# Kernel optimization log

Measured on AMD Instinct MI355X. Metric: run time of the kernel, lower is better.

## Reference

```python
import jax, jax.numpy as jnp
import numpy as np

B, T, H, FUT = 256, 512, 128, 512


def setup_inputs() -> dict:
    key = jax.random.key(0)
    ks = jax.random.split(key, 24)
    s = 1.0 / np.sqrt(H)

    def u(k, shape, scale):
        return jax.random.uniform(k, shape, jnp.float32, -scale, scale)

    inp = {
        "input": jax.random.normal(ks[0], (B, T), jnp.float32),
        "future": FUT,
        # LSTMCell 1 (input size 1)
        "Wih1": u(ks[1], (4 * H, 1), s), "Whh1": u(ks[2], (4 * H, H), s),
        "bih1": u(ks[3], (4 * H,), s), "bhh1": u(ks[4], (4 * H,), s),
        # LSTMCell 2
        "Wih2": u(ks[5], (4 * H, H), s), "Whh2": u(ks[6], (4 * H, H), s),
        "bih2": u(ks[7], (4 * H,), s), "bhh2": u(ks[8], (4 * H,), s),
        # LSTMCell 3
        "Wih3": u(ks[9], (4 * H, H), s), "Whh3": u(ks[10], (4 * H, H), s),
        "bih3": u(ks[11], (4 * H,), s), "bhh3": u(ks[12], (4 * H,), s),
        # MultiheadAttention packed in-proj (q,k,v) and out-proj
        "in_proj_w": u(ks[13], (3 * H, H), s), "in_proj_b": u(ks[14], (3 * H,), s),
        "out_w": u(ks[15], (H, H), s), "out_b": u(ks[16], (H,), s),
        # final Linear(H, 1)
        "lin_w": u(ks[17], (1, H), s), "lin_b": u(ks[18], (1,), s),
    }
    return inp


def _lstm_cell(x, h, c, Wih, Whh, bih, bhh):
    # torch LSTMCell gate order: i, f, g, o
    g = x @ Wih.T + h @ Whh.T + (bih + bhh)
    i, f, gg, o = jnp.split(g, 4, axis=-1)
    c_new = jax.nn.sigmoid(f) * c + jax.nn.sigmoid(i) * jnp.tanh(gg)
    h_new = jax.nn.sigmoid(o) * jnp.tanh(c_new)
    return h_new, c_new


def _forward(input, Wih1, Whh1, bih1, bhh1, Wih2, Whh2, bih2, bhh2,
             Wih3, Whh3, bih3, bhh3, in_proj_w, in_proj_b, out_w, out_b,
             lin_w, lin_b, future):
    hd = in_proj_w.shape[1]
    # seq_len == 1 attention: softmax over a single key is 1, so
    # attn_output = out_proj(v_proj(h3)); q/k play no role in the output.
    Wv = in_proj_w[2 * hd:]
    bv = in_proj_b[2 * hd:]

    def head(h3):
        attn = (h3 @ Wv.T + bv) @ out_w.T + out_b
        return attn @ lin_w.T + lin_b  # [B, 1]

    def step(states, x_t):
        h1, c1, h2, c2, h3, c3 = states
        h1, c1 = _lstm_cell(x_t, h1, c1, Wih1, Whh1, bih1, bhh1)
        h2, c2 = _lstm_cell(h1, h2, c2, Wih2, Whh2, bih2, bhh2)
        h3, c3 = _lstm_cell(h2, h3, c3, Wih3, Whh3, bih3, bhh3)
        return (h1, c1, h2, c2, h3, c3), head(h3)

    n = input.shape[0]
    z = jnp.zeros((n, hd), input.dtype)
    init = (z, z, z, z, z, z)

    xs = input.T[:, :, None]  # [T, B, 1]
    states, outs = jax.lax.scan(lambda s, x: step(s, x), init, xs)

    def fstep(carry, _):
        st, out = carry
        st, out = step(st, out)
        return (st, out), out

    (_, _), fouts = jax.lax.scan(fstep, (states, outs[-1]), None, length=future)
    all_outs = jnp.concatenate([outs, fouts], axis=0)  # [T+future, B, 1]
    return all_outs[..., 0].T  # [B, T+future]


def reference(input, Wih1, Whh1, bih1, bhh1, Wih2, Whh2, bih2, bhh2,
              Wih3, Whh3, bih3, bhh3, in_proj_w, in_proj_b, out_w, out_b,
              lin_w, lin_b, future):
    return _forward(input, Wih1, Whh1, bih1, bhh1, Wih2, Whh2, bih2, bhh2,
                    Wih3, Whh3, bih3, bhh3, in_proj_w, in_proj_b, out_w,
                    out_b, lin_w, lin_b, future)
```

## Files before the change

kernel.cpp:

```cpp
#include <hip/hip_runtime.h>


typedef _Float16 f16;
typedef _Float16 f16x2 __attribute__((ext_vector_type(2)));
typedef unsigned int u32;

#define T_IN 512
#define T_TOT 1024
#define NBLK 128

__device__ __forceinline__ f16x2 u2h(u32 u) { return __builtin_bit_cast(f16x2, u); }

__device__ __forceinline__ float fdot2f(f16x2 a, f16x2 b, float c) {
#if __has_builtin(__builtin_amdgcn_fdot2)
  return __builtin_amdgcn_fdot2(a, b, c, false);
#else
  return c + (float)a[0] * (float)b[0] + (float)a[1] * (float)b[1];
#endif
}

__device__ __forceinline__ float frcp(float x) {
#if __has_builtin(__builtin_amdgcn_rcpf)
  return __builtin_amdgcn_rcpf(x);
#else
  return 1.f / x;
#endif
}
__device__ __forceinline__ float fsigm(float x) { return frcp(1.f + __expf(-x)); }
__device__ __forceinline__ float ftanh(float x) { return 1.f - 2.f * frcp(1.f + __expf(2.f * x)); }

#define DOT4(acc, w, hv)                     \
  do {                                       \
    f16x2 _h = u2h(hv);                      \
    acc[0] = fdot2f(u2h((w).x), _h, acc[0]); \
    acc[1] = fdot2f(u2h((w).y), _h, acc[1]); \
    acc[2] = fdot2f(u2h((w).z), _h, acc[2]); \
    acc[3] = fdot2f(u2h((w).w), _h, acc[3]); \
  } while (0)

__global__ void pack_cat(u32* dst, const float* A, const float* Bm, int Pa, int P) {
  int tid = blockIdx.x * 256 + threadIdx.x;
  if (tid >= P * 512) return;
  int g = tid & 3;
  int idx = (tid >> 2) & 127;
  int p = tid >> 9;
  int j = g * 128 + idx;
  const float* src;
  int k;
  if (p < Pa) { src = A; k = 2 * p; } else { src = Bm; k = 2 * (p - Pa); }
  union { f16 h[2]; u32 u; } cv;
  cv.h[0] = (f16)src[j * 128 + k];
  cv.h[1] = (f16)src[j * 128 + k + 1];
  dst[tid] = cv.u;
}

__global__ void pack1(u32* dst, const float* Whh1) {
  int tid = blockIdx.x * 256 + threadIdx.x;
  if (tid >= 64 * 512) return;
  int g = tid & 3;
  int idx = (tid >> 2) & 127;
  int p = tid >> 9;
  int j = g * 128 + idx;
  union { f16 h[2]; u32 u; } cv;
  cv.h[0] = (f16)Whh1[j * 128 + 2 * p];
  cv.h[1] = (f16)Whh1[j * 128 + 2 * p + 1];
  dst[(p * 128 + (idx ^ (2 * (p >> 4)))) * 4 + g] = cv.u;
}

__global__ void pack3(u32* dst, const float* Wih3, const float* Whh3) {
  int tid = blockIdx.x * 256 + threadIdx.x;
  if (tid >= 128 * 512) return;
  int g = tid & 3;
  int u4i = tid >> 2;
  int kq = u4i & 3;
  int idx = (u4i >> 2) & 127;
  int i = u4i >> 9;
  int p = (i < 16) ? (64 + kq * 16 + i) : (kq * 16 + (i - 16));
  int j = g * 128 + idx;
  const float* src = (p < 64) ? Wih3 : Whh3;
  int k = (p < 64) ? 2 * p : 2 * (p - 64);
  union { f16 h[2]; u32 u; } cv;
  cv.h[0] = (f16)src[j * 128 + k];
  cv.h[1] = (f16)src[j * 128 + k + 1];
  dst[tid] = cv.u;
}

__global__ void prep_cons(float* cons, const float* a1, const float* b1,
                          const float* a2, const float* b2,
                          const float* a3, const float* b3, const float* wih1) {
  int tid = blockIdx.x * 256 + threadIdx.x;
  if (tid >= 2048) return;
  int gg = tid >> 9, g = (tid >> 7) & 3, idx = tid & 127;
  int j = g * 128 + idx;
  float v;
  if (gg == 0) v = a1[j] + b1[j];
  else if (gg == 1) v = a2[j] + b2[j];
  else if (gg == 2) v = a3[j] + b3[j];
  else v = wih1[j];
  cons[tid] = v;
}

__global__ void head_fold(float* cons, const float* lin_w, const float* out_w,
                          const float* Wv, const float* bv,
                          const float* out_b, const float* lin_b) {
  __shared__ float wlo[128];
  __shared__ float pr[128];
  int j = threadIdx.x;
  float s = 0.f;
  for (int k = 0; k < 128; ++k) s += lin_w[k] * out_w[k * 128 + j];
  wlo[j] = s;
  __syncthreads();
  float t = 0.f;
  for (int k = 0; k < 128; ++k) t += wlo[k] * Wv[k * 128 + j];
  cons[2048 + j] = t;
  pr[j] = s * bv[j] + lin_w[j] * out_b[j];
  __syncthreads();
  if (j == 0) {
    float b = lin_b[0];
    for (int k = 0; k < 128; ++k) b += pr[k];
    cons[2176] = b;
  }
}

__global__ __launch_bounds__(512, 1) void pendulum_persist(
    const float* __restrict__ input, const uint4* __restrict__ WT1g,
    const uint4* __restrict__ WT2, const uint4* __restrict__ WT3r,
    const float* __restrict__ consG, float* __restrict__ out) {
  __shared__ __align__(16) uint4 w1lds[8192];
  __shared__ __align__(16) f16 h1b[2][2][128];
  __shared__ __align__(16) f16 h2b[2][2][128];
  __shared__ __align__(16) f16 h3b[2][128];
  __shared__ float consL[2180];
  __shared__ float redp[2][8];

  const int t = threadIdx.x;
  const int idx = t >> 2;
  const int kq = t & 3;
  const int row0 = blockIdx.x * 2, row1 = row0 + 1;

  for (int e = t; e < 8192; e += 512) w1lds[e] = WT1g[e];
  for (int e = t; e < 2177; e += 512) consL[e] = consG[e];
  if (t < 128) {
    h1b[0][0][t] = (f16)0.f; h1b[0][1][t] = (f16)0.f;
    h1b[1][0][t] = (f16)0.f; h1b[1][1][t] = (f16)0.f;
    h2b[0][0][t] = (f16)0.f; h2b[0][1][t] = (f16)0.f;
    h2b[1][0][t] = (f16)0.f; h2b[1][1][t] = (f16)0.f;
    h3b[0][t] = (f16)0.f;    h3b[1][t] = (f16)0.f;
  }

  uint4 w2r[32];
#pragma unroll
  for (int j = 0; j < 32; ++j) w2r[j] = WT2[(kq * 32 + j) * 128 + idx];

  const uint4* W3p = WT3r + t;
  const uint4* w1p = w1lds + kq * 2048 + (idx ^ (2 * kq));

  float c1a = 0.f, c1b = 0.f, c2a = 0.f, c2b = 0.f, c3a = 0.f, c3b = 0.f;
  float y0 = 0.f, y1 = 0.f;
  __syncthreads();
  const float beffv = consL[2176];

  {
    float x0 = input[row0 * T_IN], x1 = input[row1 * T_IN];
    if (kq == 0) {
      float b0 = consL[idx], b1v = consL[128 + idx], b2v = consL[256 + idx],
            b3v = consL[384 + idx];
      float w0 = consL[1536 + idx], w1w = consL[1664 + idx],
            w2w = consL[1792 + idx], w3w = consL[1920 + idx];
      {
        float ig = fsigm(b0 + x0 * w0), fg = fsigm(b1v + x0 * w1w);
        float gg = ftanh(b2v + x0 * w2w), og = fsigm(b3v + x0 * w3w);
        (void)fg; c1a = ig * gg; h1b[0][0][idx] = (f16)(og * ftanh(c1a));
      }
      {
        float ig = fsigm(b0 + x1 * w0), fg = fsigm(b1v + x1 * w1w);
        float gg = ftanh(b2v + x1 * w2w), og = fsigm(b3v + x1 * w3w);
        (void)fg; c1b = ig * gg; h1b[0][1][idx] = (f16)(og * ftanh(c1b));
      }
    }
    __syncthreads();
  }

  uint4 ring[8];
#pragma unroll
  for (int c = 0; c < 8; ++c) ring[c] = W3p[c * 512];

  for (int s = 0; s < T_TOT; ++s) {
    const int par = s & 1;
    const int xi = (s + 1 < T_IN) ? (s + 1) : 0;
    float xl0 = input[row0 * T_IN + xi];
    float xl1 = input[row1 * T_IN + xi];

    const uint4* hL2r0 = (kq < 2)
        ? (const uint4*)&h1b[par][0][0] + kq * 8
        : (const uint4*)&h2b[par ^ 1][0][0] + (kq - 2) * 8;
    const uint4* hL2r1 = (kq < 2)
        ? (const uint4*)&h1b[par][1][0] + kq * 8
        : (const uint4*)&h2b[par ^ 1][1][0] + (kq - 2) * 8;
    const uint4* h3r0 = (const uint4*)&h3b[0][0] + kq * 4;
    const uint4* h3r1 = (const uint4*)&h3b[1][0] + kq * 4;

    float a2r0[4] = {0, 0, 0, 0}, a2r1[4] = {0, 0, 0, 0};
    float a3r0[4] = {0, 0, 0, 0}, a3r1[4] = {0, 0, 0, 0};

    uint4 E0, E1;
#pragma unroll
    for (int q = 0; q < 8; ++q) {
      uint4 H0 = hL2r0[q], H1 = hL2r1[q];
      u32 e0[4] = {H0.x, H0.y, H0.z, H0.w};
      u32 e1[4] = {H1.x, H1.y, H1.z, H1.w};
#pragma unroll
      for (int e = 0; e < 4; ++e) {
        uint4 w = w2r[q * 4 + e];
        DOT4(a2r0, w, e0[e]);
        DOT4(a2r1, w, e1[e]);
      }
      if ((q & 1) == 0) { E0 = h3r0[q >> 1]; E1 = h3r1[q >> 1]; }
      {
        uint4 w = ring[(2 * q) & 7];
        ring[(2 * q) & 7] = W3p[(2 * q + 8) * 512];
        u32 h0 = (q & 1) ? E0.z : E0.x, h1v = (q & 1) ? E1.z : E1.x;
        DOT4(a3r0, w, h0);
        DOT4(a3r1, w, h1v);
      }
      {
        uint4 w = ring[(2 * q + 1) & 7];
        ring[(2 * q + 1) & 7] = W3p[(2 * q + 9) * 512];
        u32 h0 = (q & 1) ? E0.w : E0.y, h1v = (q & 1) ? E1.w : E1.y;
        DOT4(a3r0, w, h0);
        DOT4(a3r1, w, h1v);
      }
    }

#pragma unroll
    for (int g = 0; g < 4; ++g) {
      a2r0[g] += __shfl_xor(a2r0[g], 1, 64); a2r0[g] += __shfl_xor(a2r0[g], 2, 64);
      a2r1[g] += __shfl_xor(a2r1[g], 1, 64); a2r1[g] += __shfl_xor(a2r1[g], 2, 64);
    }
    if (kq == 0) {
      float b0 = consL[512 + idx], b1v = consL[640 + idx],
            b2v = consL[768 + idx], b3v = consL[896 + idx];
      {
        float ig = fsigm(a2r0[0] + b0), fg = fsigm(a2r0[1] + b1v);
        float gg = ftanh(a2r0[2] + b2v), og = fsigm(a2r0[3] + b3v);
        c2a = fg * c2a + ig * gg;
        h2b[par][0][idx] = (f16)(og * ftanh(c2a));
      }
      {
        float ig = fsigm(a2r1[0] + b0), fg = fsigm(a2r1[1] + b1v);
        float gg = ftanh(a2r1[2] + b2v), og = fsigm(a2r1[3] + b3v);
        c2b = fg * c2b + ig * gg;
        h2b[par][1][idx] = (f16)(og * ftanh(c2b));
      }
    }
    asm volatile("s_waitcnt lgkmcnt(0)\n\ts_barrier" ::: "memory");

    const uint4* hLTr0 = (const uint4*)&h2b[par][0][0] + kq * 4;
    const uint4* hLTr1 = (const uint4*)&h2b[par][1][0] + kq * 4;
    const uint4* h1r0 = (const uint4*)&h1b[par][0][0] + kq * 4;
    const uint4* h1r1 = (const uint4*)&h1b[par][1][0] + kq * 4;

    float a1r0[4] = {0, 0, 0, 0}, a1r1[4] = {0, 0, 0, 0};
    uint4 L0, L1v, F0, F1;
#pragma unroll
    for (int q = 0; q < 8; ++q) {
      if ((q & 1) == 0) {
        L0 = hLTr0[q >> 1]; L1v = hLTr1[q >> 1];
        F0 = h1r0[q >> 1];  F1 = h1r1[q >> 1];
      }
      {
        uint4 w = ring[(2 * q) & 7];
        ring[(2 * q) & 7] = W3p[(((16 + 2 * q) + 8) & 31) * 512];
        u32 h0 = (q & 1) ? L0.z : L0.x, h1x = (q & 1) ? L1v.z : L1v.x;
        DOT4(a3r0, w, h0);
        DOT4(a3r1, w, h1x);
      }
      {
        uint4 w = ring[(2 * q + 1) & 7];
        ring[(2 * q + 1) & 7] = W3p[(((17 + 2 * q) + 8) & 31) * 512];
        u32 h0 = (q & 1) ? L0.w : L0.y, h1x = (q & 1) ? L1v.w : L1v.y;
        DOT4(a3r0, w, h0);
        DOT4(a3r1, w, h1x);
      }
      {
        uint4 w = w1p[(2 * q) * 128];
        u32 h0 = (q & 1) ? F0.z : F0.x, h1x = (q & 1) ? F1.z : F1.x;
        DOT4(a1r0, w, h0);
        DOT4(a1r1, w, h1x);
      }
      {
        uint4 w = w1p[(2 * q + 1) * 128];
        u32 h0 = (q & 1) ? F0.w : F0.y, h1x = (q & 1) ? F1.w : F1.y;
        DOT4(a1r0, w, h0);
        DOT4(a1r1, w, h1x);
      }
    }

#pragma unroll
    for (int g = 0; g < 4; ++g) {
      a3r0[g] += __shfl_xor(a3r0[g], 1, 64); a3r0[g] += __shfl_xor(a3r0[g], 2, 64);
      a3r1[g] += __shfl_xor(a3r1[g], 1, 64); a3r1[g] += __shfl_xor(a3r1[g], 2, 64);
      a1r0[g] += __shfl_xor(a1r0[g], 1, 64); a1r0[g] += __shfl_xor(a1r0[g], 2, 64);
      a1r1[g] += __shfl_xor(a1r1[g], 1, 64); a1r1[g] += __shfl_xor(a1r1[g], 2, 64);
    }

    float p0 = 0.f, p1 = 0.f;
    if (kq == 0) {
      float b0 = consL[1024 + idx], b1v = consL[1152 + idx],
            b2v = consL[1280 + idx], b3v = consL[1408 + idx];
      float weffr = consL[2048 + idx];
      {
        float ig = fsigm(a3r0[0] + b0), fg = fsigm(a3r0[1] + b1v);
        float gg = ftanh(a3r0[2] + b2v), og = fsigm(a3r0[3] + b3v);
        c3a = fg * c3a + ig * gg;
        float h3 = og * ftanh(c3a);
        h3b[0][idx] = (f16)h3;
        p0 = weffr * h3;
      }
      {
        float ig = fsigm(a3r1[0] + b0), fg = fsigm(a3r1[1] + b1v);
        float gg = ftanh(a3r1[2] + b2v), og = fsigm(a3r1[3] + b3v);
        c3b = fg * c3b + ig * gg;
        float h3 = og * ftanh(c3b);
        h3b[1][idx] = (f16)h3;
        p1 = weffr * h3;
      }
    }
#pragma unroll
    for (int k = 1; k < 64; k <<= 1) {
      p0 += __shfl_xor(p0, k, 64);
      p1 += __shfl_xor(p1, k, 64);
    }
    if ((t & 63) == 0) { redp[0][t >> 6] = p0; redp[1][t >> 6] = p1; }
    asm volatile("s_waitcnt lgkmcnt(0)\n\ts_barrier" ::: "memory");

    y0 = beffv; y1 = beffv;
#pragma unroll
    for (int w8 = 0; w8 < 8; ++w8) { y0 += redp[0][w8]; y1 += redp[1][w8]; }
    if (t == 0) out[row0 * T_TOT + s] = y0;
    else if (t == 1) out[row1 * T_TOT + s] = y1;

    float xv0 = (s + 1 < T_IN) ? xl0 : y0;
    float xv1 = (s + 1 < T_IN) ? xl1 : y1;
    if (kq == 0) {
      float b0 = consL[idx], b1v = consL[128 + idx], b2v = consL[256 + idx],
            b3v = consL[384 + idx];
      float w0 = consL[1536 + idx], w1w = consL[1664 + idx],
            w2w = consL[1792 + idx], w3w = consL[1920 + idx];
      {
        float ig = fsigm(a1r0[0] + b0 + xv0 * w0), fg = fsigm(a1r0[1] + b1v + xv0 * w1w);
        float gg = ftanh(a1r0[2] + b2v + xv0 * w2w), og = fsigm(a1r0[3] + b3v + xv0 * w3w);
        c1a = fg * c1a + ig * gg;
        h1b[par ^ 1][0][idx] = (f16)(og * ftanh(c1a));
      }
      {
        float ig = fsigm(a1r1[0] + b0 + xv1 * w0), fg = fsigm(a1r1[1] + b1v + xv1 * w1w);
        float gg = ftanh(a1r1[2] + b2v + xv1 * w2w), og = fsigm(a1r1[3] + b3v + xv1 * w3w);
        c1b = fg * c1b + ig * gg;
        h1b[par ^ 1][1][idx] = (f16)(og * ftanh(c1b));
      }
    }
    asm volatile("s_waitcnt lgkmcnt(0)\n\ts_barrier" ::: "memory");
  }
}

extern "C" void kernel_launch(void* const* d_in, const int* in_sizes, int n_in,
                              void* d_out, int out_size, void* d_ws, size_t ws_size,
                              hipStream_t stream) {
  const float* input = (const float*)d_in[0];
  const float* Wih1 = (const float*)d_in[2];
  const float* Whh1 = (const float*)d_in[3];
  const float* bih1 = (const float*)d_in[4];
  const float* bhh1 = (const float*)d_in[5];
  const float* Wih2 = (const float*)d_in[6];
  const float* Whh2 = (const float*)d_in[7];
  const float* bih2 = (const float*)d_in[8];
  const float* bhh2 = (const float*)d_in[9];
  const float* Wih3 = (const float*)d_in[10];
  const float* Whh3 = (const float*)d_in[11];
  const float* bih3 = (const float*)d_in[12];
  const float* bhh3 = (const float*)d_in[13];
  const float* in_proj_w = (const float*)d_in[14];
  const float* in_proj_b = (const float*)d_in[15];
  const float* out_w = (const float*)d_in[16];
  const float* out_b = (const float*)d_in[17];
  const float* lin_w = (const float*)d_in[18];
  const float* lin_b = (const float*)d_in[19];

  char* ws = (char*)d_ws;
  u32* WT1 = (u32*)(ws + (0 << 10));
  u32* WT2 = (u32*)(ws + (128 << 10));
  u32* WT3r = (u32*)(ws + (384 << 10));
  float* consG = (float*)(ws + (640 << 10));

  pack1<<<128, 256, 0, stream>>>(WT1, Whh1);
  pack_cat<<<256, 256, 0, stream>>>(WT2, Wih2, Whh2, 64, 128);
  pack3<<<256, 256, 0, stream>>>(WT3r, Wih3, Whh3);
  prep_cons<<<8, 256, 0, stream>>>(consG, bih1, bhh1, bih2, bhh2, bih3, bhh3, Wih1);
  head_fold<<<1, 128, 0, stream>>>(consG, lin_w, out_w,
                                   in_proj_w + 2 * 128 * 128, in_proj_b + 256,
                                   out_b, lin_b);

  pendulum_persist<<<NBLK, 512, 0, stream>>>(
      input, (const uint4*)WT1, (const uint4*)WT2, (const uint4*)WT3r,
      consG, (float*)d_out);
}
```

Before: 10.21 ms.

## Stream layer-2 weights from global via unified ring instead of register-resident

Layer-2 weights no longer sit in 32 registers per thread. They are interleaved with layer-3 weights into a single packed stream, read each step through a 16-entry register ring prefetch. The layer-1 LDS layout also changes to a per-thread linear order without the XOR swizzle. The aim is to free registers and unify the load schedule. The cost is roughly doubled global/L2 weight traffic per step on a latency-bound recurrent loop, and possible LDS bank conflicts from the unswizzled layout.

After: 12.79 ms. 25.2% more time.

```diff
diff --git a/kernel.cpp b/kernel.cpp
--- a/kernel.cpp
+++ b/kernel.cpp
@@ -38,50 +38,48 @@
     acc[3] = fdot2f(u2h((w).w), _h, acc[3]); \
   } while (0)
 
-__global__ void pack_cat(u32* dst, const float* A, const float* Bm, int Pa, int P) {
+__global__ void pack_stream(u32* dst, const float* Wih2, const float* Whh2,
+                            const float* Wih3, const float* Whh3) {
   int tid = blockIdx.x * 256 + threadIdx.x;
-  if (tid >= P * 512) return;
+  if (tid >= 64 * 512 * 4) return;
   int g = tid & 3;
-  int idx = (tid >> 2) & 127;
-  int p = tid >> 9;
+  int t = (tid >> 2) & 511;
+  int s = tid >> 11;
+  int idx = t >> 2, kq = t & 3;
+  const float* src;
+  int p;
+  if (s < 48) {
+    int q = s / 6, rmd = s % 6;
+    if (rmd < 4) {
+      p = kq * 32 + 4 * q + rmd;
+      if (p < 64) { src = Wih2; } else { src = Whh2; p -= 64; }
+    } else {
+      p = kq * 16 + 2 * q + (rmd - 4);
+      src = Whh3;
+    }
+  } else {
+    p = kq * 16 + (s - 48);
+    src = Wih3;
+  }
   int j = g * 128 + idx;
-  const float* src;
-  int k;
-  if (p < Pa) { src = A; k = 2 * p; } else { src = Bm; k = 2 * (p - Pa); }
   union { f16 h[2]; u32 u; } cv;
-  cv.h[0] = (f16)src[j * 128 + k];
-  cv.h[1] = (f16)src[j * 128 + k + 1];
+  cv.h[0] = (f16)src[j * 128 + 2 * p];
+  cv.h[1] = (f16)src[j * 128 + 2 * p + 1];
   dst[tid] = cv.u;
 }
 
-__global__ void pack1(u32* dst, const float* Whh1) {
+__global__ void pack1s(u32* dst, const float* Whh1) {
   int tid = blockIdx.x * 256 + threadIdx.x;
-  if (tid >= 64 * 512) return;
+  if (tid >= 16 * 512 * 4) return;
   int g = tid & 3;
-  int idx = (tid >> 2) & 127;
-  int p = tid >> 9;
+  int t = (tid >> 2) & 511;
+  int q = tid >> 11;
+  int idx = t >> 2, kq = t & 3;
+  int p = kq * 16 + q;
   int j = g * 128 + idx;
   union { f16 h[2]; u32 u; } cv;
   cv.h[0] = (f16)Whh1[j * 128 + 2 * p];
   cv.h[1] = (f16)Whh1[j * 128 + 2 * p + 1];
-  dst[(p * 128 + (idx ^ (2 * (p >> 4)))) * 4 + g] = cv.u;
-}
-
-__global__ void pack3(u32* dst, const float* Wih3, const float* Whh3) {
-  int tid = blockIdx.x * 256 + threadIdx.x;
-  if (tid >= 128 * 512) return;
-  int g = tid & 3;
-  int u4i = tid >> 2;
-  int kq = u4i & 3;
-  int idx = (u4i >> 2) & 127;
-  int i = u4i >> 9;
-  int p = (i < 16) ? (64 + kq * 16 + i) : (kq * 16 + (i - 16));
-  int j = g * 128 + idx;
-  const float* src = (p < 64) ? Wih3 : Whh3;
-  int k = (p < 64) ? 2 * p : 2 * (p - 64);
-  union { f16 h[2]; u32 u; } cv;
-  cv.h[0] = (f16)src[j * 128 + k];
-  cv.h[1] = (f16)src[j * 128 + k + 1];
   dst[tid] = cv.u;
 }
 
@@ -123,10 +121,10 @@
 }
 
 __global__ __launch_bounds__(512, 1) void pendulum_persist(
-    const float* __restrict__ input, const uint4* __restrict__ WT1g,
-    const uint4* __restrict__ WT2, const uint4* __restrict__ WT3r,
-    const float* __restrict__ consG, float* __restrict__ out) {
-  __shared__ __align__(16) uint4 w1lds[8192];
+    const float* __restrict__ input, const uint4* __restrict__ WT1s,
+    const uint4* __restrict__ WS, const float* __restrict__ consG,
+    float* __restrict__ out) {
+  __shared__ __align__(16) uint4 w1s[8192];
   __shared__ __align__(16) f16 h1b[2][2][128];
   __shared__ __align__(16) f16 h2b[2][2][128];
   __shared__ __align__(16) f16 h3b[2][128];
@@ -138,7 +136,7 @@
   const int kq = t & 3;
   const int row0 = blockIdx.x * 2, row1 = row0 + 1;
 
-  for (int e = t; e < 8192; e += 512) w1lds[e] = WT1g[e];
+  for (int e = t; e < 8192; e += 512) w1s[e] = WT1s[e];
   for (int e = t; e < 2177; e += 512) consL[e] = consG[e];
   if (t < 128) {
     h1b[0][0][t] = (f16)0.f; h1b[0][1][t] = (f16)0.f;
@@ -148,12 +146,8 @@
     h3b[0][t] = (f16)0.f;    h3b[1][t] = (f16)0.f;
   }
 
-  uint4 w2r[32];
-#pragma unroll
-  for (int j = 0; j < 32; ++j) w2r[j] = WT2[(kq * 32 + j) * 128 + idx];
-
-  const uint4* W3p = WT3r + t;
-  const uint4* w1p = w1lds + kq * 2048 + (idx ^ (2 * kq));
+  const uint4* Wp = WS + t;
+  const uint4* w1p = w1s + t;
 
   float c1a = 0.f, c1b = 0.f, c2a = 0.f, c2b = 0.f, c3a = 0.f, c3b = 0.f;
   float y0 = 0.f, y1 = 0.f;
@@ -168,22 +162,23 @@
       float w0 = consL[1536 + idx], w1w = consL[1664 + idx],
             w2w = consL[1792 + idx], w3w = consL[1920 + idx];
       {
-        float ig = fsigm(b0 + x0 * w0), fg = fsigm(b1v + x0 * w1w);
+        float ig = fsigm(b0 + x0 * w0);
         float gg = ftanh(b2v + x0 * w2w), og = fsigm(b3v + x0 * w3w);
-        (void)fg; c1a = ig * gg; h1b[0][0][idx] = (f16)(og * ftanh(c1a));
-      }
-      {
-        float ig = fsigm(b0 + x1 * w0), fg = fsigm(b1v + x1 * w1w);
+        c1a = ig * gg; h1b[0][0][idx] = (f16)(og * ftanh(c1a));
+      }
+      {
+        float ig = fsigm(b0 + x1 * w0);
         float gg = ftanh(b2v + x1 * w2w), og = fsigm(b3v + x1 * w3w);
-        (void)fg; c1b = ig * gg; h1b[0][1][idx] = (f16)(og * ftanh(c1b));
-      }
+        c1b = ig * gg; h1b[0][1][idx] = (f16)(og * ftanh(c1b));
+      }
+      (void)b1v;
     }
     __syncthreads();
   }
 
-  uint4 ring[8];
-#pragma unroll
-  for (int c = 0; c < 8; ++c) ring[c] = W3p[c * 512];
+  uint4 ring[16];
+#pragma unroll
+  for (int c = 0; c < 16; ++c) ring[c] = Wp[c * 512];
 
   for (int s = 0; s < T_TOT; ++s) {
     const int par = s & 1;
@@ -209,23 +204,27 @@
       uint4 H0 = hL2r0[q], H1 = hL2r1[q];
       u32 e0[4] = {H0.x, H0.y, H0.z, H0.w};
       u32 e1[4] = {H1.x, H1.y, H1.z, H1.w};
-#pragma unroll
-      for (int e = 0; e < 4; ++e) {
-        uint4 w = w2r[q * 4 + e];
-        DOT4(a2r0, w, e0[e]);
-        DOT4(a2r1, w, e1[e]);
-      }
       if ((q & 1) == 0) { E0 = h3r0[q >> 1]; E1 = h3r1[q >> 1]; }
-      {
-        uint4 w = ring[(2 * q) & 7];
-        ring[(2 * q) & 7] = W3p[(2 * q + 8) * 512];
+#pragma unroll
+      for (int m = 0; m < 4; ++m) {
+        const int sl = 6 * q + m;
+        uint4 w = ring[sl & 15];
+        ring[sl & 15] = Wp[((sl + 16) & 63) * 512];
+        DOT4(a2r0, w, e0[m]);
+        DOT4(a2r1, w, e1[m]);
+      }
+      {
+        const int sl = 6 * q + 4;
+        uint4 w = ring[sl & 15];
+        ring[sl & 15] = Wp[((sl + 16) & 63) * 512];
         u32 h0 = (q & 1) ? E0.z : E0.x, h1v = (q & 1) ? E1.z : E1.x;
         DOT4(a3r0, w, h0);
         DOT4(a3r1, w, h1v);
       }
       {
-        uint4 w = ring[(2 * q + 1) & 7];
-        ring[(2 * q + 1) & 7] = W3p[(2 * q + 9) * 512];
+        const int sl = 6 * q + 5;
+        uint4 w = ring[sl & 15];
+        ring[sl & 15] = Wp[((sl + 16) & 63) * 512];
         u32 h0 = (q & 1) ? E0.w : E0.y, h1v = (q & 1) ? E1.w : E1.y;
         DOT4(a3r0, w, h0);
         DOT4(a3r1, w, h1v);
@@ -269,27 +268,29 @@
         F0 = h1r0[q >> 1];  F1 = h1r1[q >> 1];
       }
       {
-        uint4 w = ring[(2 * q) & 7];
-        ring[(2 * q) & 7] = W3p[(((16 + 2 * q) + 8) & 31) * 512];
+        const int sl = 48 + 2 * q;
+        uint4 w = ring[sl & 15];
+        ring[sl & 15] = Wp[((sl + 16) & 63) * 512];
         u32 h0 = (q & 1) ? L0.z : L0.x, h1x = (q & 1) ? L1v.z : L1v.x;
         DOT4(a3r0, w, h0);
         DOT4(a3r1, w, h1x);
       }
       {
-        uint4 w = ring[(2 * q + 1) & 7];
-        ring[(2 * q + 1) & 7] = W3p[(((17 + 2 * q) + 8) & 31) * 512];
+        const int sl = 48 + 2 * q + 1;
+        uint4 w = ring[sl & 15];
+        ring[sl & 15] = Wp[((sl + 16) & 63) * 512];
         u32 h0 = (q & 1) ? L0.w : L0.y, h1x = (q & 1) ? L1v.w : L1v.y;
         DOT4(a3r0, w, h0);
         DOT4(a3r1, w, h1x);
       }
       {
-        uint4 w = w1p[(2 * q) * 128];
+        uint4 w = w1p[(2 * q) * 512];
         u32 h0 = (q & 1) ? F0.z : F0.x, h1x = (q & 1) ? F1.z : F1.x;
         DOT4(a1r0, w, h0);
         DOT4(a1r1, w, h1x);
       }
       {
-        uint4 w = w1p[(2 * q + 1) * 128];
+        uint4 w = w1p[(2 * q + 1) * 512];
         u32 h0 = (q & 1) ? F0.w : F0.y, h1x = (q & 1) ? F1.w : F1.y;
         DOT4(a1r0, w, h0);
         DOT4(a1r1, w, h1x);
@@ -388,20 +389,17 @@
   const float* lin_b = (const float*)d_in[19];
 
   char* ws = (char*)d_ws;
-  u32* WT1 = (u32*)(ws + (0 << 10));
-  u32* WT2 = (u32*)(ws + (128 << 10));
-  u32* WT3r = (u32*)(ws + (384 << 10));
+  u32* WT1s = (u32*)(ws + (0 << 10));
+  u32* WS = (u32*)(ws + (128 << 10));
   float* consG = (float*)(ws + (640 << 10));
 
-  pack1<<<128, 256, 0, stream>>>(WT1, Whh1);
-  pack_cat<<<256, 256, 0, stream>>>(WT2, Wih2, Whh2, 64, 128);
-  pack3<<<256, 256, 0, stream>>>(WT3r, Wih3, Whh3);
+  pack1s<<<128, 256, 0, stream>>>(WT1s, Whh1);
+  pack_stream<<<512, 256, 0, stream>>>(WS, Wih2, Whh2, Wih3, Whh3);
   prep_cons<<<8, 256, 0, stream>>>(consG, bih1, bhh1, bih2, bhh2, bih3, bhh3, Wih1);
   head_fold<<<1, 128, 0, stream>>>(consG, lin_w, out_w,
                                    in_proj_w + 2 * 128 * 128, in_proj_b + 256,
                                    out_b, lin_b);
 
   pendulum_persist<<<NBLK, 512, 0, stream>>>(
-      input, (const uint4*)WT1, (const uint4*)WT2, (const uint4*)WT3r,
-      consG, (float*)d_out);
-}
+      input, (const uint4*)WT1s, (const uint4*)WS, consG, (float*)d_out);
+}
```
